# Optimization experiments

Measured on AMD Instinct MI355X. Metric: run time of the kernel, lower is better.

The kernel has to match this reference:

```python
import jax, jax.numpy as jnp
import numpy as np

B, T, C, H = 8, 1024, 768, 12
D = C // H  # head_dim = 64

def _rope_tables(seq_len, d, base=10000.0):
    inv_freq = 1.0 / (base ** (jnp.arange(0, d, 2, dtype=jnp.float32) / d))  # [d/2]
    freqs = jnp.outer(jnp.arange(seq_len, dtype=jnp.float32), inv_freq)      # [T, d/2]
    return jnp.cos(freqs), jnp.sin(freqs)

def _apply_rotary(x, cos, sin):
    # x: [B,T,H,D]; cos/sin: [1,T,1,D/2]
    d = x.shape[-1] // 2
    x1, x2 = x[..., :d], x[..., d:]
    return jnp.concatenate([x1 * cos + x2 * sin, -x1 * sin + x2 * cos], axis=-1)

def setup_inputs() -> dict:
    key = jax.random.key(0)
    k1, k2, k3 = jax.random.split(key, 3)
    x = jax.random.normal(k1, (B, T, C), dtype=jnp.float32)
    w_qkv = jax.random.normal(k2, (3 * C, C), dtype=jnp.float32) * (C ** -0.5)
    w_proj = jax.random.normal(k3, (C, C), dtype=jnp.float32) * (C ** -0.5)
    return {"x": x, "w_qkv": w_qkv, "w_proj": w_proj}

def reference(x, w_qkv, w_proj):
    Bb, Tt, Cc = x.shape
    qkv = x @ w_qkv.T                                   # [B,T,3C]
    q, k, v = jnp.split(qkv, 3, axis=2)
    q = q.reshape(Bb, Tt, H, D)
    k = k.reshape(Bb, Tt, H, D)
    v = v.reshape(Bb, Tt, H, D)
    cos, sin = _rope_tables(Tt, D)
    cos = cos[None, :, None, :]
    sin = sin[None, :, None, :]
    q = _apply_rotary(q, cos, sin)
    k = _apply_rotary(k, cos, sin)
    scale = 1.0 / jnp.sqrt(jnp.float32(D))
    scores = jnp.einsum('bthd,bshd->bhts', q, k) * scale  # [B,H,T,T]
    causal = jnp.tril(jnp.ones((Tt, Tt), dtype=bool))
    scores = jnp.where(causal[None, None], scores, jnp.finfo(scores.dtype).min)
    p = jax.nn.softmax(scores, axis=-1)
    y = jnp.einsum('bhts,bshd->bthd', p, v).reshape(Bb, Tt, Cc)
    return y @ w_proj.T
```

## Files before the change

kernel.cpp:

```cpp
#include <hip/hip_runtime.h>
#include <hip/hip_bf16.h>

#define Bb 8
#define Tt 1024
#define Cc 768
#define Hh 12
#define Dd 64
#define M_ROWS (Bb * Tt)
#define QKV_N (3 * Cc)

typedef __attribute__((ext_vector_type(8))) short s16x8;
typedef __attribute__((ext_vector_type(4))) short s16x4;
typedef __attribute__((ext_vector_type(4))) float f32x4;

#define AS1 __attribute__((address_space(1)))
#define AS3 __attribute__((address_space(3)))

static __device__ __forceinline__ short f2bf(float f) {
    union { float f; unsigned u; } v; v.f = f;
    unsigned r = (v.u + 0x7fffu + ((v.u >> 16) & 1u)) >> 16;
    return (short)r;
}
static __device__ __forceinline__ unsigned pkt(float hi, float lo) {
    union { float f; unsigned u; } a, b; a.f = hi; b.f = lo;
    return __builtin_amdgcn_perm(a.u, b.u, 0x07060302u);
}

static __device__ __forceinline__ void cast8(const float* __restrict__ in,
                                             short* __restrict__ out, int i) {
    const float4 a = ((const float4*)in)[i * 2];
    const float4 b = ((const float4*)in)[i * 2 + 1];
    s16x8 f;
    f[0] = f2bf(a.x); f[1] = f2bf(a.y); f[2] = f2bf(a.z); f[3] = f2bf(a.w);
    f[4] = f2bf(b.x); f[5] = f2bf(b.y); f[6] = f2bf(b.z); f[7] = f2bf(b.w);
    ((s16x8*)out)[i] = f;
}

#define S1 (M_ROWS * Cc / 8)
#define S2 (QKV_N * Cc / 8)
#define S3 (Cc * Cc / 8)
#define SROPE (Tt * 32)
#define PREP_THREADS (S1 + S2 + S3 + SROPE)

__global__ __launch_bounds__(256) void prep_kernel(const float* __restrict__ x,
                                                   const float* __restrict__ wqkv,
                                                   const float* __restrict__ wproj,
                                                   short* __restrict__ xb,
                                                   short* __restrict__ wqkvb,
                                                   short* __restrict__ wprojb,
                                                   float2* __restrict__ cs) {
    int idx = blockIdx.x * blockDim.x + threadIdx.x;
    if (idx < S1) { cast8(x, xb, idx); return; }
    idx -= S1;
    if (idx < S2) { cast8(wqkv, wqkvb, idx); return; }
    idx -= S2;
    if (idx < S3) { cast8(wproj, wprojb, idx); return; }
    idx -= S3;
    {
        int t = idx >> 5, i = idx & 31;
        float inv_freq = exp2f(-0.41524101186092037f * (float)i);
        float fr = (float)t * inv_freq;
        float2 v; v.x = cosf(fr); v.y = sinf(fr);
        cs[idx] = v;
    }
}

template <int MODE, int TN>
__global__ __launch_bounds__(256, 3) void gemm_nt_mfma(const short* __restrict__ A,
                                                       const short* __restrict__ B,
                                                       void* __restrict__ Cout,
                                                       const float2* __restrict__ cs,
                                                       int M, int N, int K, int nblocks) {
    __shared__ short As[2][128 * 32];
    __shared__ short Bs[2][TN * 32];
    constexpr int NT = TN / 16;

    const int wave = threadIdx.x >> 6;
    const int lane = threadIdx.x & 63;
    const int l16  = lane & 15;
    const int quad = lane >> 4;

    const int mb8  = (M >> 7) >> 3;
    const int xcd  = blockIdx.x & 7;
    const int slot = blockIdx.x >> 3;
    const int bm = (xcd * mb8 + slot / nblocks) * 128;
    const int bn = (slot % nblocks) * TN;

    f32x4 acc[2][NT] = {};

    auto stage = [&](int k0, int buf) {
#pragma unroll
        for (int j = 0; j < 2; j++) {
            const int D = j * 256 + wave * 64 + lane;
            const int G = D >> 3;
            const int s = (G << 3) | ((D & 7) ^ (G & 7));
            const int m = s >> 2, c4 = (s & 3) * 8;
            __builtin_amdgcn_global_load_lds(
                (const AS1 unsigned*)(A + (size_t)(bm + m) * K + k0 + c4),
                (AS3 unsigned*)&As[buf][(j * 256 + wave * 64) * 8], 16, 0, 0);
        }
        constexpr int BCH = TN * 4;
#pragma unroll
        for (int j = 0; j < (BCH + 255) / 256; j++) {
            if (BCH % 256 == 0 || j * 256 + wave * 64 < BCH) {
                const int D = j * 256 + wave * 64 + lane;
                const int G = D >> 3;
                const int s = (G << 3) | ((D & 7) ^ (G & 7));
                const int m = s >> 2, c4 = (s & 3) * 8;
                __builtin_amdgcn_global_load_lds(
                    (const AS1 unsigned*)(B + (size_t)(bn + m) * K + k0 + c4),
                    (AS3 unsigned*)&Bs[buf][(j * 256 + wave * 64) * 8], 16, 0, 0);
            }
        }
    };

    const int nIter = K >> 5;
    stage(0, 0);
    for (int kt = 0; kt < nIter; kt++) {
        const int buf = kt & 1;
        __syncthreads();
        if (kt + 1 < nIter) stage((kt + 1) << 5, buf ^ 1);

        s16x8 af[2];
#pragma unroll
        for (int mt = 0; mt < 2; mt++) {
            const int m = wave * 32 + mt * 16 + l16;
            const int d = ((m & 1) * 4 + quad) ^ ((m >> 1) & 7);
            af[mt] = *(const s16x8*)&As[buf][(m >> 1) * 64 + d * 8];
        }
#pragma unroll
        for (int nt = 0; nt < NT; nt++) {
            const int n = nt * 16 + l16;
            const int d = ((n & 1) * 4 + quad) ^ ((n >> 1) & 7);
            s16x8 bf = *(const s16x8*)&Bs[buf][(n >> 1) * 64 + d * 8];
            acc[0][nt] = __builtin_amdgcn_mfma_f32_16x16x32_bf16(af[0], bf, acc[0][nt], 0, 0, 0);
            acc[1][nt] = __builtin_amdgcn_mfma_f32_16x16x32_bf16(af[1], bf, acc[1][nt], 0, 0, 0);
        }
    }

    if constexpr (MODE == 0) {
#pragma unroll
        for (int mt = 0; mt < 2; mt++)
#pragma unroll
            for (int r = 0; r < 4; r++) {
                const size_t row = bm + wave * 32 + mt * 16 + quad * 4 + r;
#pragma unroll
                for (int nt = 0; nt < NT; nt++)
                    ((float*)Cout)[row * N + bn + nt * 16 + l16] = acc[mt][nt][r];
            }
    } else {
        const bool is_v = (bn >= 2 * Cc);
        if (is_v) {
#pragma unroll
            for (int mt = 0; mt < 2; mt++)
#pragma unroll
                for (int r = 0; r < 4; r++) {
                    const size_t row = bm + wave * 32 + mt * 16 + quad * 4 + r;
#pragma unroll
                    for (int nt = 0; nt < NT; nt++)
                        ((short*)Cout)[row * N + bn + nt * 16 + l16] = f2bf(acc[mt][nt][r]);
                }
        } else {
            const float scale = (bn < Cc) ? 0.125f : 1.0f;
#pragma unroll
            for (int mt = 0; mt < 2; mt++) {
#pragma unroll
                for (int r = 0; r < 4; r++) {
                    const int row = bm + wave * 32 + mt * 16 + quad * 4 + r;
                    const int t = row & (Tt - 1);
                    const float2 c0 = cs[t * 32 + l16];
                    const float2 c1 = cs[t * 32 + 16 + l16];
#pragma unroll
                    for (int hh = 0; hh < TN / 64; hh++) {
                        const float x0 = acc[mt][hh * 4 + 0][r];
                        const float x1 = acc[mt][hh * 4 + 1][r];
                        const float x2 = acc[mt][hh * 4 + 2][r];
                        const float x3 = acc[mt][hh * 4 + 3][r];
                        short* cp = (short*)Cout + (size_t)row * N + bn + hh * 64;
                        cp[l16]      = f2bf((x0 * c0.x + x2 * c0.y) * scale);
                        cp[16 + l16] = f2bf((x1 * c1.x + x3 * c1.y) * scale);
                        cp[32 + l16] = f2bf((-x0 * c0.y + x2 * c0.x) * scale);
                        cp[48 + l16] = f2bf((-x1 * c1.y + x3 * c1.x) * scale);
                    }
                }
            }
        }
    }
}

#define KSP 72
#define VSP 72

__global__ __launch_bounds__(256, 3) void flash_attn(const short* __restrict__ qkv,
                                                     short* __restrict__ y) {
    __shared__ short Ks[2][64 * KSP];
    __shared__ short Vs[2][64 * VSP];

    const int wave = threadIdx.x >> 6;
    const int lane = threadIdx.x & 63;
    const int l16  = lane & 15;
    const int quad = lane >> 4;

    const int pair = blockIdx.x / 96;
    const int bh   = blockIdx.x % 96;
    const int h = bh % Hh;
    const int b = bh / Hh;
    const int qa_blk = pair;
    const int qb_blk = 15 - pair;
    const int q0a = qa_blk * 64 + wave * 16;
    const int q0b = qb_blk * 64 + wave * 16;

    s16x8 qfa[2], qfb[2];
    {
        const short* qpa = qkv + (size_t)(b * Tt + q0a + l16) * QKV_N + h * Dd + quad * 8;
        const short* qpb = qkv + (size_t)(b * Tt + q0b + l16) * QKV_N + h * Dd + quad * 8;
        qfa[0] = *(const s16x8*)qpa;  qfa[1] = *(const s16x8*)(qpa + 32);
        qfb[0] = *(const s16x8*)qpb;  qfb[1] = *(const s16x8*)(qpb + 32);
    }

    f32x4 oa[4] = {}, ob[4] = {};
    float la = 0.f, lb = 0.f;

    const int krow = threadIdx.x >> 2;
    const int kd0  = (threadIdx.x & 3) * 16;
    const int key2 = (threadIdx.x & 31) * 2;
    const int dv0  = (threadIdx.x >> 5) * 8;

    s16x8 pk0, pk1, pv0, pv1;
    auto load_tile = [&](int kbase) {
        const short* kp = qkv + (size_t)(b * Tt + kbase + krow) * QKV_N + Cc + h * Dd + kd0;
        pk0 = *(const s16x8*)kp;
        pk1 = *(const s16x8*)(kp + 8);
        const short* vp = qkv + (size_t)(b * Tt + kbase + key2) * QKV_N + 2 * Cc + h * Dd + dv0;
        pv0 = *(const s16x8*)vp;
        pv1 = *(const s16x8*)(vp + QKV_N);
    };
    auto store_tile = [&](int buf) {
        *(s16x8*)&Ks[buf][krow * KSP + kd0]     = pk0;
        *(s16x8*)&Ks[buf][krow * KSP + kd0 + 8] = pk1;
#pragma unroll
        for (int j = 0; j < 8; j++) {
            ushort2 w; w.x = (unsigned short)pv0[j]; w.y = (unsigned short)pv1[j];
            *(ushort2*)&Vs[buf][(dv0 + j) * VSP + key2] = w;
        }
    };

    auto process_pair = [&](int buf, int kbase, bool mask_a) {
        short* pwb = &Ks[buf ^ 1][wave * 16 * KSP];
        short* pwa = &Vs[buf ^ 1][wave * 16 * VSP];
        f32x4 eb[4], ea[4];
#pragma unroll
        for (int g = 0; g < 4; g++) {
            s16x8 kf0 = *(const s16x8*)&Ks[buf][(g * 16 + l16) * KSP + quad * 8];
            s16x8 kf1 = *(const s16x8*)&Ks[buf][(g * 16 + l16) * KSP + 32 + quad * 8];
            f32x4 zb = {}, za = {};
            zb = __builtin_amdgcn_mfma_f32_16x16x32_bf16(kf0, qfb[0], zb, 0, 0, 0);
            zb = __builtin_amdgcn_mfma_f32_16x16x32_bf16(kf1, qfb[1], zb, 0, 0, 0);
            za = __builtin_amdgcn_mfma_f32_16x16x32_bf16(kf0, qfa[0], za, 0, 0, 0);
            za = __builtin_amdgcn_mfma_f32_16x16x32_bf16(kf1, qfa[1], za, 0, 0, 0);
            eb[g] = zb; ea[g] = za;
        }
        float rsb = 0.f, rsa = 0.f;
#pragma unroll
        for (int g = 0; g < 4; g++) {
#pragma unroll
            for (int r = 0; r < 4; r++) {
                float pb = __expf(eb[g][r]); rsb += pb; eb[g][r] = pb;
                float pa = __expf(ea[g][r]);
                if (mask_a) pa = (kbase + g * 16 + quad * 4 + r <= q0a + l16) ? pa : 0.0f;
                rsa += pa; ea[g][r] = pa;
            }
            uint2 ub, ua;
            ub.x = pkt(eb[g][1], eb[g][0]); ub.y = pkt(eb[g][3], eb[g][2]);
            ua.x = pkt(ea[g][1], ea[g][0]); ua.y = pkt(ea[g][3], ea[g][2]);
            *(uint2*)&pwb[l16 * KSP + g * 16 + quad * 4] = ub;
            *(uint2*)&pwa[l16 * VSP + g * 16 + quad * 4] = ua;
        }
        lb += rsb; la += rsa;
#pragma unroll
        for (int c = 0; c < 2; c++) {
            s16x8 pbb = *(const s16x8*)&pwb[l16 * KSP + c * 32 + quad * 8];
            s16x8 pba = *(const s16x8*)&pwa[l16 * VSP + c * 32 + quad * 8];
#pragma unroll
            for (int nc = 0; nc < 4; nc++) {
                s16x8 vb = *(const s16x8*)&Vs[buf][(nc * 16 + l16) * VSP + c * 32 + quad * 8];
                ob[nc] = __builtin_amdgcn_mfma_f32_16x16x32_bf16(vb, pbb, ob[nc], 0, 0, 0);
                oa[nc] = __builtin_amdgcn_mfma_f32_16x16x32_bf16(vb, pba, oa[nc], 0, 0, 0);
            }
        }
    };

    auto process_single = [&](int buf, int kbase, bool masked) {
        short* pw = &Ks[buf ^ 1][wave * 16 * KSP];
        f32x4 e[4];
#pragma unroll
        for (int g = 0; g < 4; g++) {
            s16x8 kf0 = *(const s16x8*)&Ks[buf][(g * 16 + l16) * KSP + quad * 8];
            s16x8 kf1 = *(const s16x8*)&Ks[buf][(g * 16 + l16) * KSP + 32 + quad * 8];
            f32x4 z = {};
            z = __builtin_amdgcn_mfma_f32_16x16x32_bf16(kf0, qfb[0], z, 0, 0, 0);
            z = __builtin_amdgcn_mfma_f32_16x16x32_bf16(kf1, qfb[1], z, 0, 0, 0);
            e[g] = z;
        }
        float rs = 0.f;
#pragma unroll
        for (int g = 0; g < 4; g++) {
#pragma unroll
            for (int r = 0; r < 4; r++) {
                float p = __expf(e[g][r]);
                if (masked) p = (kbase + g * 16 + quad * 4 + r <= q0b + l16) ? p : 0.0f;
                rs += p; e[g][r] = p;
            }
            uint2 u;
            u.x = pkt(e[g][1], e[g][0]); u.y = pkt(e[g][3], e[g][2]);
            *(uint2*)&pw[l16 * KSP + g * 16 + quad * 4] = u;
        }
        lb += rs;
#pragma unroll
        for (int c = 0; c < 2; c++) {
            s16x8 pb = *(const s16x8*)&pw[l16 * KSP + c * 32 + quad * 8];
#pragma unroll
            for (int nc = 0; nc < 4; nc++) {
                s16x8 vb = *(const s16x8*)&Vs[buf][(nc * 16 + l16) * VSP + c * 32 + quad * 8];
                ob[nc] = __builtin_amdgcn_mfma_f32_16x16x32_bf16(vb, pb, ob[nc], 0, 0, 0);
            }
        }
    };

    load_tile(0);
    store_tile(0);
    for (int kt = 0; kt <= qb_blk; kt++) {
        __syncthreads();
        const int nb = (kt < qb_blk) ? (kt + 1) * 64 : qb_blk * 64;
        load_tile(nb);
        const int buf = kt & 1;
        const int kbase = kt * 64;
        if (kt <= qa_blk)
            process_pair(buf, kbase, kt == qa_blk);
        else
            process_single(buf, kbase, kt == qb_blk);
        store_tile(buf ^ 1);
    }

    float sa = la; sa += __shfl_xor(sa, 16, 64); sa += __shfl_xor(sa, 32, 64);
    float sb = lb; sb += __shfl_xor(sb, 16, 64); sb += __shfl_xor(sb, 32, 64);
    const float inva = 1.0f / sa;
    const float invb = 1.0f / sb;
    short* ypa = y + (size_t)(b * Tt + q0a + l16) * Cc + h * Dd + quad * 4;
    short* ypb = y + (size_t)(b * Tt + q0b + l16) * Cc + h * Dd + quad * 4;
#pragma unroll
    for (int nc = 0; nc < 4; nc++) {
        s16x4 va, vb2;
#pragma unroll
        for (int r = 0; r < 4; r++) {
            va[r]  = f2bf(oa[nc][r] * inva);
            vb2[r] = f2bf(ob[nc][r] * invb);
        }
        *(s16x4*)&ypa[nc * 16] = va;
        *(s16x4*)&ypb[nc * 16] = vb2;
    }
}

extern "C" void kernel_launch(void* const* d_in, const int* in_sizes, int n_in,
                              void* d_out, int out_size, void* d_ws, size_t ws_size,
                              hipStream_t stream) {
    const float* x      = (const float*)d_in[0];
    const float* w_qkv  = (const float*)d_in[1];
    const float* w_proj = (const float*)d_in[2];
    float* out = (float*)d_out;

    float2* cs    = (float2*)d_ws;
    short* xb     = (short*)(cs + Tt * 32);
    short* wqkvb  = xb + (size_t)M_ROWS * Cc;
    short* wprojb = wqkvb + (size_t)QKV_N * Cc;
    short* qkvb   = wprojb + (size_t)Cc * Cc;
    short* yb     = qkvb + (size_t)M_ROWS * QKV_N;

    prep_kernel<<<PREP_THREADS / 256, 256, 0, stream>>>(
        x, w_qkv, w_proj, xb, wqkvb, wprojb, cs);

    gemm_nt_mfma<1, 192><<<768, 256, 0, stream>>>(
        xb, wqkvb, qkvb, cs, M_ROWS, QKV_N, Cc, QKV_N / 192);

    flash_attn<<<96 * 8, 256, 0, stream>>>(qkvb, yb);

    gemm_nt_mfma<0, 96><<<512, 256, 0, stream>>>(
        yb, wprojb, out, nullptr, M_ROWS, Cc, Cc, Cc / 96);
}
```

Measured before the change: 168.1 us.

## Use 2x2 wave tiling in GEMM and permute QKV weight rows for local RoPE

The GEMM's four waves now form a 2x2 grid, each computing a 64xTN/2 sub-tile, instead of each wave owning 32 rows across the full TN width. This increases fragment reuse: each B fragment feeds four MFMAs rather than two, which cuts LDS reads per MFMA. To keep RoPE pairs inside one wave's column half, the prep kernel permutes the Q/K rows of the weight matrix (swapping 16-row groups within each head), so the rotary pairs land in adjacent accumulator tiles. The cost is a more complex epilogue and a dependence on an exact weight-row permutation.

```diff
diff --git a/kernel.cpp b/kernel.cpp
--- a/kernel.cpp
+++ b/kernel.cpp
@@ -52,7 +52,19 @@
     int idx = blockIdx.x * blockDim.x + threadIdx.x;
     if (idx < S1) { cast8(x, xb, idx); return; }
     idx -= S1;
-    if (idx < S2) { cast8(wqkv, wqkvb, idx); return; }
+    if (idx < S2) {
+        int row = idx / 96;
+        int c8  = idx - row * 96;
+        int q2 = (row >> 4) & 3;
+        int src = (row < 2 * Cc && (q2 == 1 || q2 == 2)) ? (row ^ 0x30) : row;
+        const float4 a = ((const float4*)(wqkv + (size_t)src * Cc))[c8 * 2];
+        const float4 b = ((const float4*)(wqkv + (size_t)src * Cc))[c8 * 2 + 1];
+        s16x8 f;
+        f[0] = f2bf(a.x); f[1] = f2bf(a.y); f[2] = f2bf(a.z); f[3] = f2bf(a.w);
+        f[4] = f2bf(b.x); f[5] = f2bf(b.y); f[6] = f2bf(b.z); f[7] = f2bf(b.w);
+        ((s16x8*)wqkvb)[idx] = f;
+        return;
+    }
     idx -= S2;
     if (idx < S3) { cast8(wproj, wprojb, idx); return; }
     idx -= S3;
@@ -73,12 +85,14 @@
                                                        int M, int N, int K, int nblocks) {
     __shared__ short As[2][128 * 32];
     __shared__ short Bs[2][TN * 32];
-    constexpr int NT = TN / 16;
+    constexpr int NTW = TN / 32;
 
     const int wave = threadIdx.x >> 6;
     const int lane = threadIdx.x & 63;
     const int l16  = lane & 15;
     const int quad = lane >> 4;
+    const int wr = wave >> 1;
+    const int wc = wave & 1;
 
     const int mb8  = (M >> 7) >> 3;
     const int xcd  = blockIdx.x & 7;
@@ -86,7 +100,7 @@
     const int bm = (xcd * mb8 + slot / nblocks) * 128;
     const int bn = (slot % nblocks) * TN;
 
-    f32x4 acc[2][NT] = {};
+    f32x4 acc[4][NTW] = {};
 
     auto stage = [&](int k0, int buf) {
 #pragma unroll
@@ -121,66 +135,67 @@
         __syncthreads();
         if (kt + 1 < nIter) stage((kt + 1) << 5, buf ^ 1);
 
-        s16x8 af[2];
-#pragma unroll
-        for (int mt = 0; mt < 2; mt++) {
-            const int m = wave * 32 + mt * 16 + l16;
+        s16x8 af[4];
+#pragma unroll
+        for (int mt = 0; mt < 4; mt++) {
+            const int m = wr * 64 + mt * 16 + l16;
             const int d = ((m & 1) * 4 + quad) ^ ((m >> 1) & 7);
             af[mt] = *(const s16x8*)&As[buf][(m >> 1) * 64 + d * 8];
         }
 #pragma unroll
-        for (int nt = 0; nt < NT; nt++) {
-            const int n = nt * 16 + l16;
+        for (int nt = 0; nt < NTW; nt++) {
+            const int n = wc * (TN / 2) + nt * 16 + l16;
             const int d = ((n & 1) * 4 + quad) ^ ((n >> 1) & 7);
             s16x8 bf = *(const s16x8*)&Bs[buf][(n >> 1) * 64 + d * 8];
-            acc[0][nt] = __builtin_amdgcn_mfma_f32_16x16x32_bf16(af[0], bf, acc[0][nt], 0, 0, 0);
-            acc[1][nt] = __builtin_amdgcn_mfma_f32_16x16x32_bf16(af[1], bf, acc[1][nt], 0, 0, 0);
+#pragma unroll
+            for (int mt = 0; mt < 4; mt++)
+                acc[mt][nt] = __builtin_amdgcn_mfma_f32_16x16x32_bf16(
+                    af[mt], bf, acc[mt][nt], 0, 0, 0);
         }
     }
 
     if constexpr (MODE == 0) {
 #pragma unroll
-        for (int mt = 0; mt < 2; mt++)
+        for (int mt = 0; mt < 4; mt++)
 #pragma unroll
             for (int r = 0; r < 4; r++) {
-                const size_t row = bm + wave * 32 + mt * 16 + quad * 4 + r;
-#pragma unroll
-                for (int nt = 0; nt < NT; nt++)
-                    ((float*)Cout)[row * N + bn + nt * 16 + l16] = acc[mt][nt][r];
+                const size_t row = bm + wr * 64 + mt * 16 + quad * 4 + r;
+#pragma unroll
+                for (int nt = 0; nt < NTW; nt++)
+                    ((float*)Cout)[row * N + bn + wc * (TN / 2) + nt * 16 + l16] =
+                        acc[mt][nt][r];
             }
     } else {
         const bool is_v = (bn >= 2 * Cc);
         if (is_v) {
 #pragma unroll
-            for (int mt = 0; mt < 2; mt++)
+            for (int mt = 0; mt < 4; mt++)
 #pragma unroll
                 for (int r = 0; r < 4; r++) {
-                    const size_t row = bm + wave * 32 + mt * 16 + quad * 4 + r;
-#pragma unroll
-                    for (int nt = 0; nt < NT; nt++)
-                        ((short*)Cout)[row * N + bn + nt * 16 + l16] = f2bf(acc[mt][nt][r]);
+                    const size_t row = bm + wr * 64 + mt * 16 + quad * 4 + r;
+#pragma unroll
+                    for (int nt = 0; nt < NTW; nt++)
+                        ((short*)Cout)[row * N + bn + wc * (TN / 2) + nt * 16 + l16] =
+                            f2bf(acc[mt][nt][r]);
                 }
         } else {
             const float scale = (bn < Cc) ? 0.125f : 1.0f;
 #pragma unroll
-            for (int mt = 0; mt < 2; mt++) {
+            for (int mt = 0; mt < 4; mt++) {
 #pragma unroll
                 for (int r = 0; r < 4; r++) {
-                    const int row = bm + wave * 32 + mt * 16 + quad * 4 + r;
+                    const int row = bm + wr * 64 + mt * 16 + quad * 4 + r;
                     const int t = row & (Tt - 1);
-                    const float2 c0 = cs[t * 32 + l16];
-                    const float2 c1 = cs[t * 32 + 16 + l16];
-#pragma unroll
-                    for (int hh = 0; hh < TN / 64; hh++) {
-                        const float x0 = acc[mt][hh * 4 + 0][r];
-                        const float x1 = acc[mt][hh * 4 + 1][r];
-                        const float x2 = acc[mt][hh * 4 + 2][r];
-                        const float x3 = acc[mt][hh * 4 + 3][r];
-                        short* cp = (short*)Cout + (size_t)row * N + bn + hh * 64;
-                        cp[l16]      = f2bf((x0 * c0.x + x2 * c0.y) * scale);
-                        cp[16 + l16] = f2bf((x1 * c1.x + x3 * c1.y) * scale);
-                        cp[32 + l16] = f2bf((-x0 * c0.y + x2 * c0.x) * scale);
-                        cp[48 + l16] = f2bf((-x1 * c1.y + x3 * c1.x) * scale);
+                    short* cp = (short*)Cout + (size_t)row * N + bn + wc * (TN / 2);
+#pragma unroll
+                    for (int p = 0; p < NTW; p += 2) {
+                        const int g = wc * NTW + p;
+                        const int i0 = ((g & 2) ? 16 : 0) + l16;
+                        const float2 c0 = cs[t * 32 + i0];
+                        const float x1 = acc[mt][p][r];
+                        const float x2 = acc[mt][p + 1][r];
+                        cp[p * 16 + l16]        = f2bf((x1 * c0.x + x2 * c0.y) * scale);
+                        cp[(p + 1) * 16 + l16]  = f2bf((-x1 * c0.y + x2 * c0.x) * scale);
                     }
                 }
             }
```

Measured after the change: 167.9 us. About the same (-0.2%).
